# Optimization experiments

Measured on AMD Instinct MI355X. Metric: run time of the kernel, lower is better.

Reference implementation:

```python
import jax, jax.numpy as jnp
import numpy as np

HEAD_N = 16
EMBED_D = 1024
MASK_FILL = 1e-09  # source uses masked_fill(mask==0, 1e-09), NOT -inf


def setup_inputs() -> dict:
    key = jax.random.key(0)
    ks = jax.random.split(key, 8)
    B, S, D = 4, 4096, EMBED_D
    L = S // HEAD_N
    q = jax.random.normal(ks[0], (B, S, D), dtype=jnp.float32)
    k = jax.random.normal(ks[1], (B, S, D), dtype=jnp.float32)
    v = jax.random.normal(ks[2], (B, S, D), dtype=jnp.float32)
    mask = jax.random.randint(ks[3], (B, L, L), 0, 2, dtype=jnp.int32)
    scale = 0.02
    Wq = jax.random.normal(ks[4], (D, D), dtype=jnp.float32) * scale
    Wk = jax.random.normal(ks[5], (D, D), dtype=jnp.float32) * scale
    Wv = jax.random.normal(ks[6], (D, D), dtype=jnp.float32) * scale
    Wo = jax.random.normal(ks[7], (D, D), dtype=jnp.float32) * scale
    return {"q": q, "k": k, "v": v, "mask": mask, "Wq": Wq, "Wk": Wk, "Wv": Wv, "Wo": Wo}


def _split_heads(x, B):
    # Faithful to source bug: view(B, -1, head_n, embedding_d).transpose(1, 2)
    # -> splits the SEQUENCE dim by head_n; per-head dim stays EMBED_D.
    return x.reshape(B, -1, HEAD_N, EMBED_D).transpose(0, 2, 1, 3)  # [B,h,L,D]


def reference(q, k, v, mask, Wq, Wk, Wv, Wo):
    B, S, D = q.shape
    qh = _split_heads(q @ Wq, B)
    kh = _split_heads(k @ Wk, B)
    vh = _split_heads(v @ Wv, B)
    # score: [B, h, L, L], L = S // head_n
    score = jnp.einsum("bhld,bhmd->bhlm", qh, kh) / jnp.sqrt(jnp.float32(D))
    m = mask[:, None, :, :]  # unsqueeze(1) -> broadcast over heads
    score = jnp.where(m == 0, jnp.float32(MASK_FILL), score)
    att = jax.nn.softmax(score, axis=-1)  # dropout p=0.0 -> identity
    x = jnp.einsum("bhlm,bhmd->bhld", att, vh)  # [B,h,L,D]
    x = x.transpose(0, 2, 1, 3).reshape(B, S, D)
    return x @ Wo
```

## Files before the change

### kernel.cpp

```cpp
#include <hip/hip_runtime.h>
#include <hip/hip_bf16.h>

typedef __bf16 bf16x8 __attribute__((ext_vector_type(8)));
typedef float f32x4 __attribute__((ext_vector_type(4)));
typedef unsigned short ushort_t;
typedef unsigned int uint_t;

#define HN 16
#define LSEQ 256
#define DD 1024
#define BB 4
#define SS 4096
#define MROWS (BB * SS)
#define BHN (BB * HN)

__device__ __forceinline__ ushort_t f2bf(float f) {
  uint_t u = __builtin_bit_cast(uint_t, f);
  u += 0x7fffu + ((u >> 16) & 1u);
  return (ushort_t)(u >> 16);
}
__device__ __forceinline__ uint_t cvtpk(float lo, float hi) {
  uint_t r;
  asm("v_cvt_pk_bf16_f32 %0, %1, %2" : "=v"(r) : "v"(lo), "v"(hi));
  return r;
}

__global__ __launch_bounds__(256) void transpose_w4(const float* __restrict__ W0,
                                                    const float* __restrict__ W1,
                                                    const float* __restrict__ W2,
                                                    const float* __restrict__ W3,
                                                    ushort_t* __restrict__ WT) {
  __shared__ float tile[32][33];
  const int z = blockIdx.z;
  const float* W = (z == 0) ? W0 : (z == 1) ? W1 : (z == 2) ? W2 : W3;
  ushort_t* dst = WT + (long)z * 1048576;
  const int tx = threadIdx.x, ty = threadIdx.y;
  const int bn = blockIdx.x * 32, bk = blockIdx.y * 32;
#pragma unroll
  for (int j = 0; j < 32; j += 8)
    tile[ty + j][tx] = W[(long)(bk + ty + j) * DD + bn + tx];
  __syncthreads();
#pragma unroll
  for (int j = 0; j < 32; j += 8)
    dst[(long)(bn + ty + j) * DD + bk + tx] = f2bf(tile[tx][ty + j]);
}

__global__ __launch_bounds__(256) void transpose_v(const ushort_t* __restrict__ vh,
                                                   ushort_t* __restrict__ vhT) {
  __shared__ ushort_t tile[32][33];
  const int tx = threadIdx.x, ty = threadIdx.y;
  const long zo = (long)blockIdx.z * (LSEQ * DD);
  const ushort_t* src = vh + zo;
  ushort_t* dst = vhT + zo;
  const int bd = blockIdx.x * 32;
  const int bl = blockIdx.y * 32;
#pragma unroll
  for (int j = 0; j < 32; j += 8)
    tile[ty + j][tx] = src[(long)(bl + ty + j) * DD + bd + tx];
  __syncthreads();
#pragma unroll
  for (int j = 0; j < 32; j += 8)
    dst[(long)(bd + ty + j) * LSEQ + bl + tx] = tile[tx][ty + j];
}

__global__ __launch_bounds__(256, 2) void score_sm(const ushort_t* __restrict__ qh,
                                                   const ushort_t* __restrict__ kh,
                                                   const int* __restrict__ mask,
                                                   ushort_t* __restrict__ att) {
  __shared__ char smemraw[81920];
  ushort_t* sA = (ushort_t*)smemraw;
  ushort_t* sB = (ushort_t*)(smemraw + 16384);
  float* Sf = (float*)smemraw;

  const int orig = blockIdx.x;
  const int wgid = (orig & 7) * 32 + (orig >> 3);
  const int bh = wgid >> 2, rb = wgid & 3;
  const int b = bh >> 4;
  const ushort_t* A = qh + ((long)bh * 256 + rb * 64) * 1024;
  const ushort_t* Bk = kh + (long)bh * 256 * 1024;

  const int t = threadIdx.x, lane = t & 63, wid = t >> 6;
  const int fr = lane & 15, q = lane >> 4;
  const int wc = wid * 64;
  const int sw0 = (q ^ (fr & 7)) * 8;
  const int sw1 = ((4 + q) ^ (fr & 7)) * 8;

  int srcAo[2], dstA[2], srcBo[8], dstB[8];
#pragma unroll
  for (int i = 0; i < 2; ++i) {
    const int c = i * 256 + t, row = c >> 3, gc = (c & 7) ^ (row & 7);
    srcAo[i] = row * 1024 + gc * 8;
    dstA[i] = (i * 256 + (t & 192)) * 8;
  }
#pragma unroll
  for (int i = 0; i < 8; ++i) {
    const int c = i * 256 + t, row = c >> 3, gc = (c & 7) ^ (row & 7);
    srcBo[i] = row * 1024 + gc * 8;
    dstB[i] = (i * 256 + (t & 192)) * 8;
  }

  auto stage = [&](int buf, int kt) {
    const int ko = kt * 64;
#pragma unroll
    for (int i = 0; i < 2; ++i)
      __builtin_amdgcn_global_load_lds(
          (const __attribute__((address_space(1))) void*)(A + srcAo[i] + ko),
          (__attribute__((address_space(3))) void*)(sA + buf * 4096 + dstA[i]), 16, 0, 0);
#pragma unroll
    for (int i = 0; i < 8; ++i)
      __builtin_amdgcn_global_load_lds(
          (const __attribute__((address_space(1))) void*)(Bk + srcBo[i] + ko),
          (__attribute__((address_space(3))) void*)(sB + buf * 16384 + dstB[i]), 16, 0, 0);
  };

  f32x4 acc[4][4];
#pragma unroll
  for (int m = 0; m < 4; ++m)
#pragma unroll
    for (int n = 0; n < 4; ++n) acc[m][n] = (f32x4){0.f, 0.f, 0.f, 0.f};

  stage(0, 0);
  __syncthreads();
  int cur = 0;
  for (int kt = 0; kt < 16; ++kt) {
    if (kt < 15) stage(cur ^ 1, kt + 1);
    bf16x8 af[4][2], bfv[4][2];
    const ushort_t* bA = sA + cur * 4096;
    const ushort_t* bB = sB + cur * 16384;
#pragma unroll
    for (int m = 0; m < 4; ++m) {
      af[m][0] = *(const bf16x8*)(bA + (m * 16 + fr) * 64 + sw0);
      af[m][1] = *(const bf16x8*)(bA + (m * 16 + fr) * 64 + sw1);
    }
#pragma unroll
    for (int n = 0; n < 4; ++n) {
      bfv[n][0] = *(const bf16x8*)(bB + (wc + n * 16 + fr) * 64 + sw0);
      bfv[n][1] = *(const bf16x8*)(bB + (wc + n * 16 + fr) * 64 + sw1);
    }
#pragma unroll
    for (int m = 0; m < 4; ++m)
#pragma unroll
      for (int n = 0; n < 4; ++n) {
        acc[m][n] = __builtin_amdgcn_mfma_f32_16x16x32_bf16(af[m][0], bfv[n][0], acc[m][n], 0, 0, 0);
        acc[m][n] = __builtin_amdgcn_mfma_f32_16x16x32_bf16(af[m][1], bfv[n][1], acc[m][n], 0, 0, 0);
      }
    __syncthreads();
    cur ^= 1;
  }

#pragma unroll
  for (int m = 0; m < 4; ++m)
#pragma unroll
    for (int n = 0; n < 4; ++n)
#pragma unroll
      for (int r = 0; r < 4; ++r)
        Sf[(m * 16 + q * 4 + r) * 256 + wc + n * 16 + fr] = acc[m][n][r];
  __syncthreads();

#pragma unroll 2
  for (int i = 0; i < 16; ++i) {
    const int row = wid * 16 + i;
    const int gl = rb * 64 + row;
    const f32x4 sv = *(const f32x4*)&Sf[row * 256 + lane * 4];
    const int4 mv = *(const int4*)&mask[((long)b * 256 + gl) * 256 + lane * 4];
    float s[4];
    s[0] = (mv.x == 0) ? 1e-9f : sv[0] * 0.03125f;
    s[1] = (mv.y == 0) ? 1e-9f : sv[1] * 0.03125f;
    s[2] = (mv.z == 0) ? 1e-9f : sv[2] * 0.03125f;
    s[3] = (mv.w == 0) ? 1e-9f : sv[3] * 0.03125f;
    float mx = fmaxf(fmaxf(s[0], s[1]), fmaxf(s[2], s[3]));
#pragma unroll
    for (int off = 32; off; off >>= 1) mx = fmaxf(mx, __shfl_xor(mx, off));
    float e[4], sum = 0.f;
#pragma unroll
    for (int j = 0; j < 4; ++j) {
      e[j] = __expf(s[j] - mx);
      sum += e[j];
    }
#pragma unroll
    for (int off = 32; off; off >>= 1) sum += __shfl_xor(sum, off);
    const float inv = 1.0f / sum;
    ushort4 o;
    o.x = f2bf(e[0] * inv);
    o.y = f2bf(e[1] * inv);
    o.z = f2bf(e[2] * inv);
    o.w = f2bf(e[3] * inv);
    *(ushort4*)&att[((long)bh * 256 + gl) * 256 + lane * 4] = o;
  }
}

template <int SMODE>
__global__ __launch_bounds__(256, 2) void gemm_tn(const ushort_t* __restrict__ Ab,
                                                  const ushort_t* __restrict__ Btp,
                                                  void* __restrict__ Cp, int K, int ldA,
                                                  int ldB, int ldC, long batchA,
                                                  long batchB, long batchC) {
  __shared__ ushort_t smem[16384];
  ushort_t* sA = smem;
  ushort_t* sB = smem + 8192;

  const int bx = blockIdx.x, by = blockIdx.y, z = blockIdx.z;
  const int rowBase = by * 128;
  const int colBase = bx * 128;

  const int t = threadIdx.x;
  const int lane = t & 63;
  const int wid = t >> 6;
  const int wr = (wid >> 1) * 64;
  const int wc = (wid & 1) * 64;
  const int fr = lane & 15;
  const int fk = (lane >> 4) * 8;

  const ushort_t* Atile = Ab + batchA * z + (long)rowBase * ldA;
  const ushort_t* Btile = Btp + batchB * z + (long)colBase * ldB;

  f32x4 acc[4][4];
#pragma unroll
  for (int m = 0; m < 4; ++m)
#pragma unroll
    for (int n = 0; n < 4; ++n) acc[m][n] = (f32x4){0.f, 0.f, 0.f, 0.f};

  const int NT = K >> 5;

  auto stageAB = [&](int buf, int kt) {
    const long ko = (long)kt * 32;
#pragma unroll
    for (int i = 0; i < 2; ++i) {
      const int c = i * 256 + t;
      const int cw = i * 256 + (t & 192);
      __builtin_amdgcn_global_load_lds(
          (const __attribute__((address_space(1))) void*)(Atile + (long)(c >> 2) * ldA + ko +
                                                          (c & 3) * 8),
          (__attribute__((address_space(3))) void*)(sA + buf * 4096 + cw * 8), 16, 0, 0);
      __builtin_amdgcn_global_load_lds(
          (const __attribute__((address_space(1))) void*)(Btile + (long)(c >> 2) * ldB + ko +
                                                          (c & 3) * 8),
          (__attribute__((address_space(3))) void*)(sB + buf * 4096 + cw * 8), 16, 0, 0);
    }
  };

  stageAB(0, 0);
  __syncthreads();

  int cur = 0;
  for (int kt = 0; kt < NT; ++kt) {
    if (kt + 1 < NT) stageAB(cur ^ 1, kt + 1);

    bf16x8 af[4], bfv[4];
    const ushort_t* baseA = sA + cur * 4096 + fk;
    const ushort_t* baseB = sB + cur * 4096 + fk;
#pragma unroll
    for (int m = 0; m < 4; ++m) af[m] = *(const bf16x8*)(baseA + (wr + m * 16 + fr) * 32);
#pragma unroll
    for (int n = 0; n < 4; ++n) bfv[n] = *(const bf16x8*)(baseB + (wc + n * 16 + fr) * 32);

#pragma unroll
    for (int m = 0; m < 4; ++m)
#pragma unroll
      for (int n = 0; n < 4; ++n)
        acc[m][n] = __builtin_amdgcn_mfma_f32_16x16x32_bf16(af[m], bfv[n], acc[m][n], 0, 0, 0);

    __syncthreads();
    cur ^= 1;
  }

  const int rq = (lane >> 4) * 4;
  {
#pragma unroll
    for (int m = 0; m < 4; ++m)
#pragma unroll
      for (int n = 0; n < 4; ++n)
#pragma unroll
        for (int r = 0; r < 4; ++r)
          smem[(wr + m * 16 + rq + r) * 128 + wc + n * 16 + fr] = f2bf(acc[m][n][r]);
    __syncthreads();
    ushort_t* Cb = (ushort_t*)Cp;
    const int c8 = (lane & 15) * 8;
#pragma unroll
    for (int i = 0; i < 8; ++i) {
      const int row = i * 16 + wid * 4 + (lane >> 4);
      const uint4 val = *(const uint4*)(smem + row * 128 + c8);
      const int l = rowBase + row;
      const int orow = ((z >> 4) << 12) + l * 16 + (z & 15);
      *(uint4*)(Cb + (long)orow * 1024 + colBase + c8) = val;
    }
  }
}

#define SBAR() asm volatile("s_barrier" ::: "memory")
#define LGKM0() asm volatile("s_waitcnt lgkmcnt(0)" ::: "memory")
#define VM(N) asm volatile("s_waitcnt vmcnt(" #N ")" ::: "memory")

template <int SMODE>
__global__ __launch_bounds__(512, 1) void gemm256(const ushort_t* __restrict__ A0,
                                                  const ushort_t* __restrict__ Btp,
                                                  void* __restrict__ Cp) {
  __shared__ ushort_t sm[65536];

  const int orig = blockIdx.x;
  const int cpx = (int)gridDim.x >> 3;
  const int wgid = (orig & 7) * cpx + (orig >> 3);
  const int by = wgid >> 2, bx = wgid & 3;
  const int rowBase = by * 256, colBase = bx * 256;

  const ushort_t* Ab = A0;
  const ushort_t* Bt = Btp;

  const int t = threadIdx.x;
  const int lane = t & 63;
  const int wid = t >> 6;
  const int wm = wid >> 2;
  const int wn = wid & 3;
  const int fr = lane & 15;
  const int q = lane >> 4;

  const int sw0 = ((q ^ (fr & 7)) * 8);
  const int sw1 = (((4 + q) ^ (fr & 7)) * 8);
  const int aoff0 = fr * 64 + sw0;
  const int aoff1 = fr * 64 + sw1;
  const int bbase = ((wn & 1) * 64 + fr) * 64;
  const int boff0 = bbase + sw0;
  const int boff1 = bbase + sw1;

  const ushort_t* srcA[2][2];
  const ushort_t* srcB[2][2];
  int ldsoff[2];
#pragma unroll
  for (int i = 0; i < 2; ++i) {
    const int c = i * 512 + t;
    const int rowc = c >> 3;
    const int gc = (c & 7) ^ (rowc & 7);
    srcA[0][i] = Ab + (long)(rowBase + rowc) * 1024 + gc * 8;
    srcA[1][i] = Ab + (long)(rowBase + 128 + rowc) * 1024 + gc * 8;
    srcB[0][i] = Bt + (long)(colBase + rowc) * 1024 + gc * 8;
    srcB[1][i] = Bt + (long)(colBase + 128 + rowc) * 1024 + gc * 8;
    ldsoff[i] = (c & ~63) * 8;
  }

#define STAGE(kind, h, T)                                                                   \
  do {                                                                                      \
    ushort_t* _d = sm + ((kind) ? 32768 : 0) + ((T) & 1) * 16384 + (h) * 8192;              \
    const ushort_t* _s0 = ((kind) ? srcB[h][0] : srcA[h][0]) + (long)(T) * 64;              \
    __builtin_amdgcn_global_load_lds((const __attribute__((address_space(1))) void*)_s0,    \
                                     (__attribute__((address_space(3))) void*)(_d + ldsoff[0]), \
                                     16, 0, 0);                                             \
    const ushort_t* _s1 = ((kind) ? srcB[h][1] : srcA[h][1]) + (long)(T) * 64;              \
    __builtin_amdgcn_global_load_lds((const __attribute__((address_space(1))) void*)_s1,    \
                                     (__attribute__((address_space(3))) void*)(_d + ldsoff[1]), \
                                     16, 0, 0);                                             \
  } while (0)

  f32x4 acc[8][4];
#pragma unroll
  for (int m = 0; m < 8; ++m)
#pragma unroll
    for (int n = 0; n < 4; ++n) acc[m][n] = (f32x4){0.f, 0.f, 0.f, 0.f};

  bf16x8 af[4][2], bf0[2][2], bf1[2][2];

#define LDA4(dbuf, msub)                                                         \
  do {                                                                           \
    const ushort_t* _b = sm + (dbuf)*16384 + wm * 8192 + (msub)*4096;            \
    _Pragma("unroll") for (int m2 = 0; m2 < 4; ++m2) {                           \
      af[m2][0] = *(const bf16x8*)(_b + m2 * 1024 + aoff0);                      \
      af[m2][1] = *(const bf16x8*)(_b + m2 * 1024 + aoff1);                      \
    }                                                                            \
  } while (0)

#define LDB2(dbuf, nsub, bfv)                                                    \
  do {                                                                           \
    const ushort_t* _b = sm + 32768 + (dbuf)*16384 + (wn >> 1) * 8192 + (nsub)*2048; \
    _Pragma("unroll") for (int n2 = 0; n2 < 2; ++n2) {                           \
      bfv[n2][0] = *(const bf16x8*)(_b + n2 * 1024 + boff0);                     \
      bfv[n2][1] = *(const bf16x8*)(_b + n2 * 1024 + boff1);                     \
    }                                                                            \
  } while (0)

#define MMQ(msub, nsub, bfv)                                                     \
  do {                                                                           \
    _Pragma("unroll") for (int m2 = 0; m2 < 4; ++m2)                             \
        _Pragma("unroll") for (int n2 = 0; n2 < 2; ++n2) {                       \
      acc[(msub)*4 + m2][(nsub)*2 + n2] = __builtin_amdgcn_mfma_f32_16x16x32_bf16( \
          af[m2][0], bfv[n2][0], acc[(msub)*4 + m2][(nsub)*2 + n2], 0, 0, 0);    \
      acc[(msub)*4 + m2][(nsub)*2 + n2] = __builtin_amdgcn_mfma_f32_16x16x32_bf16( \
          af[m2][1], bfv[n2][1], acc[(msub)*4 + m2][(nsub)*2 + n2], 0, 0, 0);    \
    }                                                                            \
  } while (0)

#define PH_OPEN() SBAR(); LGKM0(); __builtin_amdgcn_s_setprio(1)
#define PH_CLOSE() __builtin_amdgcn_s_setprio(0); SBAR()

  const int NT = 16;
  const int NI = 8;

  STAGE(0, 0, 0);
  STAGE(0, 1, 0);
  STAGE(1, 0, 0);
  STAGE(1, 1, 0);
  STAGE(0, 0, 1);
  VM(2);
  SBAR();

  for (int it = 0; it < NI - 1; ++it) {
    const int T0 = 2 * it;
    LDA4(0, 0);
    LDB2(0, 0, bf0);
    STAGE(0, 1, T0 + 1);
    PH_OPEN(); MMQ(0, 0, bf0); PH_CLOSE();
    LDB2(0, 1, bf1);
    STAGE(1, 0, T0 + 1);
    PH_OPEN(); MMQ(0, 1, bf1); PH_CLOSE();
    LDA4(0, 1);
    STAGE(1, 1, T0 + 1);
    PH_OPEN(); MMQ(1, 1, bf1); PH_CLOSE();
    STAGE(0, 0, T0 + 2);
    SBAR();
    __builtin_amdgcn_s_setprio(1);
    MMQ(1, 0, bf0);
    __builtin_amdgcn_s_setprio(0);
    VM(2);
    SBAR();
    LDA4(1, 0);
    LDB2(1, 0, bf0);
    STAGE(0, 1, T0 + 2);
    PH_OPEN(); MMQ(0, 0, bf0); PH_CLOSE();
    LDB2(1, 1, bf1);
    STAGE(1, 0, T0 + 2);
    PH_OPEN(); MMQ(0, 1, bf1); PH_CLOSE();
    LDA4(1, 1);
    STAGE(1, 1, T0 + 2);
    PH_OPEN(); MMQ(1, 1, bf1); PH_CLOSE();
    STAGE(0, 0, T0 + 3);
    SBAR();
    __builtin_amdgcn_s_setprio(1);
    MMQ(1, 0, bf0);
    __builtin_amdgcn_s_setprio(0);
    VM(2);
    SBAR();
  }

  {
    LDA4(0, 0);
    LDB2(0, 0, bf0);
    STAGE(0, 1, NT - 1);
    PH_OPEN(); MMQ(0, 0, bf0); PH_CLOSE();
    LDB2(0, 1, bf1);
    STAGE(1, 0, NT - 1);
    PH_OPEN(); MMQ(0, 1, bf1); PH_CLOSE();
    LDA4(0, 1);
    STAGE(1, 1, NT - 1);
    PH_OPEN(); MMQ(1, 1, bf1); PH_CLOSE();
    SBAR();
    __builtin_amdgcn_s_setprio(1);
    MMQ(1, 0, bf0);
    __builtin_amdgcn_s_setprio(0);
    VM(0);
    SBAR();
    LDA4(1, 0);
    LDB2(1, 0, bf0);
    PH_OPEN(); MMQ(0, 0, bf0); PH_CLOSE();
    LDB2(1, 1, bf1);
    PH_OPEN(); MMQ(0, 1, bf1); PH_CLOSE();
    LDA4(1, 1);
    PH_OPEN(); MMQ(1, 1, bf1); PH_CLOSE();
    SBAR();
    MMQ(1, 0, bf0);
    SBAR();
  }

  const int rq = q * 4;
  if constexpr (SMODE == 0) {
    float* Cf = (float*)Cp;
#pragma unroll
    for (int m = 0; m < 8; ++m)
#pragma unroll
      for (int n = 0; n < 4; ++n)
#pragma unroll
        for (int r = 0; r < 4; ++r) {
          const int row = rowBase + wm * 128 + m * 16 + rq + r;
          const int col = colBase + wn * 64 + n * 16 + fr;
          Cf[(long)row * 1024 + col] = acc[m][n][r];
        }
  }
#undef STAGE
}

__global__ __launch_bounds__(512, 1) void gemm256f(const float* __restrict__ A0,
                                                   const float* __restrict__ A1,
                                                   const float* __restrict__ A2,
                                                   const ushort_t* __restrict__ Btp,
                                                   ushort_t* __restrict__ Cp) {
  __shared__ ushort_t sm[65536];

  const int orig = blockIdx.x;
  const int cpx = (int)gridDim.x >> 3;
  const int wgid = (orig & 7) * cpx + (orig >> 3);
  const int z = wgid >> 8;
  const int tile = wgid & 255;
  const int by = tile >> 2, bx = tile & 3;
  const int rowBase = by * 256, colBase = bx * 256;

  const float* Af = (z == 0) ? A0 : (z == 1) ? A1 : A2;
  const ushort_t* Bt = Btp + (long)z * 1048576;

  const int t = threadIdx.x;
  const int lane = t & 63;
  const int wid = t >> 6;
  const int wm = wid >> 2;
  const int wn = wid & 3;
  const int fr = lane & 15;
  const int q = lane >> 4;

  const int sw0 = ((q ^ (fr & 7)) * 8);
  const int sw1 = (((4 + q) ^ (fr & 7)) * 8);
  const int aoff0 = fr * 64 + sw0;
  const int aoff1 = fr * 64 + sw1;
  const int bbase = ((wn & 1) * 64 + fr) * 64;
  const int boff0 = bbase + sw0;
  const int boff1 = bbase + sw1;

  const ushort_t* srcB[2][2];
  int ldsoff[2];
#pragma unroll
  for (int i = 0; i < 2; ++i) {
    const int c = i * 512 + t;
    const int rowc = c >> 3;
    const int gc = (c & 7) ^ (rowc & 7);
    srcB[0][i] = Bt + (long)(colBase + rowc) * 1024 + gc * 8;
    srcB[1][i] = Bt + (long)(colBase + 128 + rowc) * 1024 + gc * 8;
    ldsoff[i] = (c & ~63) * 8;
  }

  const int tr = t >> 2;
  const int tc = (t & 3) * 16;
  const float* aSrc[2];
  aSrc[0] = Af + (long)(rowBase + tr) * 1024 + tc;
  aSrc[1] = Af + (long)(rowBase + 128 + tr) * 1024 + tc;
  const int j0 = (t & 3) * 2;
  const int wdst0 = tr * 64 + ((j0 ^ (tr & 7)) * 8);
  const int wdst1 = tr * 64 + (((j0 + 1) ^ (tr & 7)) * 8);

  float4 rsA[4], rsB[4];

#define SB(h, T)                                                                            \
  do {                                                                                      \
    ushort_t* _d = sm + 32768 + ((T) & 1) * 16384 + (h) * 8192;                             \
    __builtin_amdgcn_global_load_lds(                                                       \
        (const __attribute__((address_space(1))) void*)(srcB[h][0] + (long)(T) * 64),       \
        (__attribute__((address_space(3))) void*)(_d + ldsoff[0]), 16, 0, 0);               \
    __builtin_amdgcn_global_load_lds(                                                       \
        (const __attribute__((address_space(1))) void*)(srcB[h][1] + (long)(T) * 64),       \
        (__attribute__((address_space(3))) void*)(_d + ldsoff[1]), 16, 0, 0);               \
  } while (0)

#define IA(rs, h, T)                                                                        \
  do {                                                                                      \
    const float* _p = aSrc[h] + (T) * 64;                                                   \
    rs[0] = *(const float4*)(_p);                                                           \
    rs[1] = *(const float4*)(_p + 4);                                                       \
    rs[2] = *(const float4*)(_p + 8);                                                       \
    rs[3] = *(const float4*)(_p + 12);                                                      \
  } while (0)

#define WA(rs, h, T)                                                                        \
  do {                                                                                      \
    ushort_t* _b = sm + ((T) & 1) * 16384 + (h) * 8192;                                     \
    uint4 _w0, _w1;                                                                         \
    _w0.x = cvtpk(rs[0].x, rs[0].y);                                                        \
    _w0.y = cvtpk(rs[0].z, rs[0].w);                                                        \
    _w0.z = cvtpk(rs[1].x, rs[1].y);                                                        \
    _w0.w = cvtpk(rs[1].z, rs[1].w);                                                        \
    _w1.x = cvtpk(rs[2].x, rs[2].y);                                                        \
    _w1.y = cvtpk(rs[2].z, rs[2].w);                                                        \
    _w1.z = cvtpk(rs[3].x, rs[3].y);                                                        \
    _w1.w = cvtpk(rs[3].z, rs[3].w);                                                        \
    *(uint4*)(_b + wdst0) = _w0;                                                            \
    *(uint4*)(_b + wdst1) = _w1;                                                            \
  } while (0)

  f32x4 acc[8][4];
#pragma unroll
  for (int m = 0; m < 8; ++m)
#pragma unroll
    for (int n = 0; n < 4; ++n) acc[m][n] = (f32x4){0.f, 0.f, 0.f, 0.f};

  bf16x8 af[4][2], bf0[2][2], bf1[2][2];

  const int NT = 16;

  IA(rsA, 0, 0);
  IA(rsB, 1, 0);
  SB(0, 0);
  SB(1, 0);
  SB(0, 1);
  SB(1, 1);
  VM(12);
  WA(rsA, 0, 0);
  VM(8);
  WA(rsB, 1, 0);
  IA(rsA, 0, 1);
  IA(rsB, 1, 1);
  VM(4);
  WA(rsA, 0, 1);
  VM(0);
  WA(rsB, 1, 1);
  LGKM0();
  SBAR();

  for (int U = 0; U < NT - 2; ++U) {
    const int d = U & 1;
    IA(rsA, 0, U + 2);
    LDA4(d, 0);
    LDB2(d, 0, bf0);
    PH_OPEN(); MMQ(0, 0, bf0); PH_CLOSE();
    LDB2(d, 1, bf1);
    SB(0, U + 1);
    PH_OPEN(); MMQ(0, 1, bf1); PH_CLOSE();
    LDA4(d, 1);
    SB(1, U + 1);
    IA(rsB, 1, U + 2);
    PH_OPEN(); MMQ(1, 1, bf1); PH_CLOSE();
    VM(8);
    WA(rsA, 0, U + 2);
    SBAR();
    __builtin_amdgcn_s_setprio(1);
    MMQ(1, 0, bf0);
    __builtin_amdgcn_s_setprio(0);
    VM(0);
    WA(rsB, 1, U + 2);
    SBAR();
  }

  {
    LDA4(0, 0);
    LDB2(0, 0, bf0);
    PH_OPEN(); MMQ(0, 0, bf0); PH_CLOSE();
    LDB2(0, 1, bf1);
    SB(0, NT - 1);
    PH_OPEN(); MMQ(0, 1, bf1); PH_CLOSE();
    LDA4(0, 1);
    SB(1, NT - 1);
    PH_OPEN(); MMQ(1, 1, bf1); PH_CLOSE();
    SBAR();
    __builtin_amdgcn_s_setprio(1);
    MMQ(1, 0, bf0);
    __builtin_amdgcn_s_setprio(0);
    VM(0);
    SBAR();
  }
  {
    LDA4(1, 0);
    LDB2(1, 0, bf0);
    PH_OPEN(); MMQ(0, 0, bf0); PH_CLOSE();
    LDB2(1, 1, bf1);
    PH_OPEN(); MMQ(0, 1, bf1); PH_CLOSE();
    LDA4(1, 1);
    PH_OPEN(); MMQ(1, 1, bf1); PH_CLOSE();
    SBAR();
    MMQ(1, 0, bf0);
    SBAR();
  }

  const int rq = q * 4;
#pragma unroll
  for (int m = 0; m < 8; ++m)
#pragma unroll
    for (int n = 0; n < 4; ++n)
#pragma unroll
      for (int r = 0; r < 4; ++r) {
        const int row = wm * 128 + m * 16 + rq + r;
        const int col = wn * 64 + n * 16 + fr;
        sm[row * 256 + (((col >> 3) ^ (row & 7)) * 8) + (col & 7)] = f2bf(acc[m][n][r]);
      }
  __syncthreads();
  ushort_t* Cb = Cp + (long)z * 16777216;
  const int cc = t & 31;
  const int r0 = t >> 5;
#pragma unroll
  for (int i = 0; i < 16; ++i) {
    const int row = r0 + i * 16;
    const uint4 val = *(const uint4*)(sm + row * 256 + ((cc ^ (row & 7)) * 8));
    const int grow = rowBase + row;
    const int b = grow >> 12;
    const int s = grow & 4095;
    const int orow = ((b << 4) + (s & 15)) * 256 + (s >> 4);
    *(uint4*)(Cb + (long)orow * 1024 + colBase + cc * 8) = val;
  }
#undef SB
#undef IA
#undef WA
#undef LDA4
#undef LDB2
#undef MMQ
#undef PH_OPEN
#undef PH_CLOSE
}

extern "C" void kernel_launch(void* const* d_in, const int* in_sizes, int n_in,
                              void* d_out, int out_size, void* d_ws, size_t ws_size,
                              hipStream_t stream) {
  const float* q = (const float*)d_in[0];
  const float* k = (const float*)d_in[1];
  const float* v = (const float*)d_in[2];
  const int* mask = (const int*)d_in[3];
  const float* Wq = (const float*)d_in[4];
  const float* Wk = (const float*)d_in[5];
  const float* Wv = (const float*)d_in[6];
  const float* Wo = (const float*)d_in[7];
  float* out = (float*)d_out;

  char* ws = (char*)d_ws;
  const size_t MB = 1024 * 1024;
  ushort_t* WT = (ushort_t*)ws;
  ushort_t* qh = (ushort_t*)(ws + 8 * MB);
  ushort_t* kh = (ushort_t*)(ws + 40 * MB);
  ushort_t* vh = (ushort_t*)(ws + 72 * MB);
  ushort_t* vhT = (ushort_t*)(ws + 104 * MB);
  ushort_t* att = (ushort_t*)(ws + 136 * MB);
  ushort_t* x = (ushort_t*)(ws + 144 * MB);

  const dim3 tb(32, 8);
  transpose_w4<<<dim3(32, 32, 4), tb, 0, stream>>>(Wq, Wk, Wv, Wo, WT);

  gemm256f<<<768, 512, 0, stream>>>(q, k, v, WT, qh);

  transpose_v<<<dim3(32, 8, BHN), tb, 0, stream>>>(vh, vhT);
  score_sm<<<256, 256, 0, stream>>>(qh, kh, mask, att);
  gemm_tn<2><<<dim3(8, 2, BHN), 256, 0, stream>>>(att, vhT, x, 256, 256, 256, 1024,
                                                  (long)65536, (long)262144, 0);
  gemm256<0><<<256, 512, 0, stream>>>(x, WT + (size_t)3145728, out);
}
```

Before: 281.6 us.

## Restructure QKV projection GEMM pipeline with ping-pong register prefetch of A tiles

Rewrites the main loop of the fp32-A projection GEMM so A-tile global loads are issued two steps ahead into alternating register sets (rsP/rsN), with bf16 conversion and LDS writes for the next tile interleaved between MFMA phases. The loop is unrolled by two with a rolled outer loop, and B async LDS loads are issued together at each iteration start. The aim is to hide global-load latency better and drop the mid-iteration waits. It doubles A staging registers, which may cut occupancy, and changes the vmcnt wait accounting, which risks ordering mistakes.

```diff
diff --git a/kernel.cpp b/kernel.cpp
--- a/kernel.cpp
+++ b/kernel.cpp
@@ -540,7 +540,7 @@
   const int wdst0 = tr * 64 + ((j0 ^ (tr & 7)) * 8);
   const int wdst1 = tr * 64 + (((j0 + 1) ^ (tr & 7)) * 8);
 
-  float4 rsA[4], rsB[4];
+  float4 rsP[8], rsN[8];
 
 #define SB(h, T)                                                                            \
   do {                                                                                      \
@@ -553,27 +553,27 @@
         (__attribute__((address_space(3))) void*)(_d + ldsoff[1]), 16, 0, 0);               \
   } while (0)
 
-#define IA(rs, h, T)                                                                        \
+#define IAh(rs, h, T)                                                                       \
   do {                                                                                      \
     const float* _p = aSrc[h] + (T) * 64;                                                   \
-    rs[0] = *(const float4*)(_p);                                                           \
-    rs[1] = *(const float4*)(_p + 4);                                                       \
-    rs[2] = *(const float4*)(_p + 8);                                                       \
-    rs[3] = *(const float4*)(_p + 12);                                                      \
+    rs[(h)*4 + 0] = *(const float4*)(_p);                                                   \
+    rs[(h)*4 + 1] = *(const float4*)(_p + 4);                                               \
+    rs[(h)*4 + 2] = *(const float4*)(_p + 8);                                               \
+    rs[(h)*4 + 3] = *(const float4*)(_p + 12);                                              \
   } while (0)
 
-#define WA(rs, h, T)                                                                        \
+#define WAh(rs, h, T)                                                                       \
   do {                                                                                      \
     ushort_t* _b = sm + ((T) & 1) * 16384 + (h) * 8192;                                     \
     uint4 _w0, _w1;                                                                         \
-    _w0.x = cvtpk(rs[0].x, rs[0].y);                                                        \
-    _w0.y = cvtpk(rs[0].z, rs[0].w);                                                        \
-    _w0.z = cvtpk(rs[1].x, rs[1].y);                                                        \
-    _w0.w = cvtpk(rs[1].z, rs[1].w);                                                        \
-    _w1.x = cvtpk(rs[2].x, rs[2].y);                                                        \
-    _w1.y = cvtpk(rs[2].z, rs[2].w);                                                        \
-    _w1.z = cvtpk(rs[3].x, rs[3].y);                                                        \
-    _w1.w = cvtpk(rs[3].z, rs[3].w);                                                        \
+    _w0.x = cvtpk(rs[(h)*4 + 0].x, rs[(h)*4 + 0].y);                                        \
+    _w0.y = cvtpk(rs[(h)*4 + 0].z, rs[(h)*4 + 0].w);                                        \
+    _w0.z = cvtpk(rs[(h)*4 + 1].x, rs[(h)*4 + 1].y);                                        \
+    _w0.w = cvtpk(rs[(h)*4 + 1].z, rs[(h)*4 + 1].w);                                        \
+    _w1.x = cvtpk(rs[(h)*4 + 2].x, rs[(h)*4 + 2].y);                                        \
+    _w1.y = cvtpk(rs[(h)*4 + 2].z, rs[(h)*4 + 2].w);                                        \
+    _w1.z = cvtpk(rs[(h)*4 + 3].x, rs[(h)*4 + 3].y);                                        \
+    _w1.w = cvtpk(rs[(h)*4 + 3].z, rs[(h)*4 + 3].w);                                        \
     *(uint4*)(_b + wdst0) = _w0;                                                            \
     *(uint4*)(_b + wdst1) = _w1;                                                            \
   } while (0)
@@ -588,58 +588,68 @@
 
   const int NT = 16;
 
-  IA(rsA, 0, 0);
-  IA(rsB, 1, 0);
+  IAh(rsP, 0, 0);
+  IAh(rsP, 1, 0);
   SB(0, 0);
   SB(1, 0);
-  SB(0, 1);
-  SB(1, 1);
-  VM(12);
-  WA(rsA, 0, 0);
+  VM(4);
+  WAh(rsP, 0, 0);
+  WAh(rsP, 1, 0);
+  IAh(rsP, 0, 1);
+  IAh(rsP, 1, 1);
   VM(8);
-  WA(rsB, 1, 0);
-  IA(rsA, 0, 1);
-  IA(rsB, 1, 1);
-  VM(4);
-  WA(rsA, 0, 1);
-  VM(0);
-  WA(rsB, 1, 1);
   LGKM0();
   SBAR();
 
-  for (int U = 0; U < NT - 2; ++U) {
-    const int d = U & 1;
-    IA(rsA, 0, U + 2);
-    LDA4(d, 0);
-    LDB2(d, 0, bf0);
-    PH_OPEN(); MMQ(0, 0, bf0); PH_CLOSE();
-    LDB2(d, 1, bf1);
-    SB(0, U + 1);
-    PH_OPEN(); MMQ(0, 1, bf1); PH_CLOSE();
-    LDA4(d, 1);
-    SB(1, U + 1);
-    IA(rsB, 1, U + 2);
-    PH_OPEN(); MMQ(1, 1, bf1); PH_CLOSE();
-    VM(8);
-    WA(rsA, 0, U + 2);
-    SBAR();
-    __builtin_amdgcn_s_setprio(1);
-    MMQ(1, 0, bf0);
-    __builtin_amdgcn_s_setprio(0);
-    VM(0);
-    WA(rsB, 1, U + 2);
-    SBAR();
+#define ITER(U, RSW, RSL, D)                                                                \
+  do {                                                                                      \
+                                                                                   \
+    VM(4);                                                            \
+    WAh(RSW, 0, (U) + 1);                                                                   \
+    SB(0, (U) + 1);                                                                         \
+    SB(1, (U) + 1);                                                                         \
+    LDA4(D, 0);                                                                             \
+    LDB2(D, 0, bf0);                                                                        \
+    PH_OPEN(); MMQ(0, 0, bf0); PH_CLOSE();                                                  \
+                                                                                   \
+    VM(4);                                                            \
+    WAh(RSW, 1, (U) + 1);                                                                   \
+    IAh(RSL, 0, (U) + 2);                                                                   \
+    LDB2(D, 1, bf1);                                                                        \
+    PH_OPEN(); MMQ(0, 1, bf1); PH_CLOSE();                                                  \
+                                                                                   \
+    LDA4(D, 1);                                                                             \
+    IAh(RSL, 1, (U) + 2);                                                                   \
+    PH_OPEN(); MMQ(1, 1, bf1); PH_CLOSE();                                                  \
+                                                                                   \
+    SBAR();                                                                                 \
+    __builtin_amdgcn_s_setprio(1);                                                          \
+    MMQ(1, 0, bf0);                                                                         \
+    __builtin_amdgcn_s_setprio(0);                                                          \
+    VM(8);                                           \
+    SBAR();                                                                                 \
+  } while (0)
+
+#pragma unroll 1
+  for (int u2 = 0; u2 < 7; ++u2) {
+    const int U0 = 2 * u2;
+    ITER(U0, rsP, rsN, 0);
+    ITER(U0 + 1, rsN, rsP, 1);
   }
 
   {
+    VM(4);
+    WAh(rsP, 0, 15);
+    SB(0, 15);
+    SB(1, 15);
     LDA4(0, 0);
     LDB2(0, 0, bf0);
     PH_OPEN(); MMQ(0, 0, bf0); PH_CLOSE();
+    VM(4);
+    WAh(rsP, 1, 15);
     LDB2(0, 1, bf1);
-    SB(0, NT - 1);
     PH_OPEN(); MMQ(0, 1, bf1); PH_CLOSE();
     LDA4(0, 1);
-    SB(1, NT - 1);
     PH_OPEN(); MMQ(1, 1, bf1); PH_CLOSE();
     SBAR();
     __builtin_amdgcn_s_setprio(1);
@@ -687,8 +697,9 @@
     *(uint4*)(Cb + (long)orow * 1024 + colBase + cc * 8) = val;
   }
 #undef SB
-#undef IA
-#undef WA
+#undef IAh
+#undef WAh
+#undef ITER
 #undef LDA4
 #undef LDB2
 #undef MMQ
```

Result: slower. 307.7 us (+9.3%).
